# Performance work log

Hardware: AMD Instinct MI355X
Metric: run time of the kernel (lower is better)

## Reference

```python
import jax, jax.numpy as jnp
import numpy as np

B, T, D, H = 64, 1024, 512, 512
_SCALE = 1.0 / np.sqrt(H)  # torch-style RNNCell init scale


def setup_inputs() -> dict:
    key = jax.random.key(0)
    ks = jax.random.split(key, 9)
    f32 = jnp.float32
    return {
        "x": jax.random.normal(ks[0], (B, T, D), dtype=f32),
        "Wih_f": jax.random.normal(ks[1], (H, D), dtype=f32) * _SCALE,
        "Whh_f": jax.random.normal(ks[2], (H, H), dtype=f32) * _SCALE,
        "bih_f": jax.random.normal(ks[3], (H,), dtype=f32) * _SCALE,
        "bhh_f": jax.random.normal(ks[4], (H,), dtype=f32) * _SCALE,
        "Wih_b": jax.random.normal(ks[5], (H, D), dtype=f32) * _SCALE,
        "Whh_b": jax.random.normal(ks[6], (H, H), dtype=f32) * _SCALE,
        "bih_b": jax.random.normal(ks[7], (H,), dtype=f32) * _SCALE,
        "bhh_b": jax.random.normal(ks[8], (H,), dtype=f32) * _SCALE,
    }


def _scan_direction(x_bt, Wih, Whh, bih, bhh):
    # x_bt: [B, T, D] already in processing order for this direction.
    # Precompute the input projection for all timesteps (one big GEMM),
    # leaving only the recurrent GEMM inside the scan.
    xp = jnp.einsum('btd,hd->bth', x_bt, Wih) + bih + bhh  # [B, T, H]
    h0 = jnp.zeros((x_bt.shape[0], Whh.shape[0]), dtype=x_bt.dtype)

    def step(h, xt):  # xt: [B, H]
        h_new = jnp.tanh(xt + h @ Whh.T)
        return h_new, h_new

    _, hs = jax.lax.scan(step, h0, jnp.swapaxes(xp, 0, 1))  # hs: [T, B, H]
    return jnp.swapaxes(hs, 0, 1)  # [B, T, H] in processing order


def reference(x, Wih_f, Whh_f, bih_f, bhh_f, Wih_b, Whh_b, bih_b, bhh_b):
    # Forward direction: timesteps 0..T-1.
    fh = _scan_direction(x, Wih_f, Whh_f, bih_f, bhh_f)
    # Backward direction: cell consumes x reversed in time; torch code appends
    # hiddens in processing order (i.e., index t <-> original time T-1-t).
    bh = _scan_direction(x[:, ::-1, :], Wih_b, Whh_b, bih_b, bhh_b)
    # output_last=False branch: [B, 2, T, H]
    return jnp.stack([fh, bh], axis=1)
```

## Files before the change

### kernel.cpp

```cpp
#include <hip/hip_runtime.h>
#include <hip/hip_fp16.h>
#include <cstdint>

typedef _Float16 h2 __attribute__((ext_vector_type(2)));
typedef _Float16 h8 __attribute__((ext_vector_type(8)));
typedef float    f2 __attribute__((ext_vector_type(2)));
typedef float    f4 __attribute__((ext_vector_type(4)));
typedef uint32_t u4 __attribute__((ext_vector_type(4)));

#define BATCH 64
#define TSTEPS 1024
#define DDIM 512
#define HDIM 512

static __device__ __forceinline__ float fdot2(uint32_t w, uint32_t h, float acc) {
  return __builtin_amdgcn_fdot2(__builtin_bit_cast(h2, w), __builtin_bit_cast(h2, h), acc, false);
}

#define BAR_LDS()                                            \
  do {                                                       \
    __builtin_amdgcn_sched_barrier(0);                       \
    asm volatile("s_waitcnt lgkmcnt(0)" ::: "memory");       \
    __builtin_amdgcn_s_barrier();                            \
    __builtin_amdgcn_sched_barrier(0);                       \
  } while (0)

__global__ void prep_kernel(const float* __restrict__ Wih_f, const float* __restrict__ Whh_f,
                            const float* __restrict__ bih_f, const float* __restrict__ bhh_f,
                            const float* __restrict__ Wih_b, const float* __restrict__ Whh_b,
                            const float* __restrict__ bih_b, const float* __restrict__ bhh_b,
                            _Float16* __restrict__ wi16, uint32_t* __restrict__ whT,
                            float* __restrict__ bsum) {
  int i = blockIdx.x * 256 + threadIdx.x;
  if (i < 2 * 512 * 512) {
    const float* s = (i < 512 * 512) ? Wih_f : Wih_b;
    wi16[i] = (_Float16)s[i & (512 * 512 - 1)];
  }
  if (i < 2 * 256 * 512) {
    int d = i >> 17; int rem = i & ((1 << 17) - 1);
    int kp = rem >> 9; int j = rem & 511;
    const float* W = d ? Whh_b : Whh_f;
    h2 p; p[0] = (_Float16)W[j * 512 + 2 * kp]; p[1] = (_Float16)W[j * 512 + 2 * kp + 1];
    whT[i] = __builtin_bit_cast(uint32_t, p);
  }
  if (i < 2 * 512) {
    int d = i >> 9, j = i & 511;
    bsum[i] = d ? (bih_b[j] + bhh_b[j]) : (bih_f[j] + bhh_f[j]);
  }
}

__global__ __launch_bounds__(256) void xp_gemm(const float* __restrict__ x,
                                               const _Float16* __restrict__ wi,
                                               const float* __restrict__ bsum,
                                               _Float16* __restrict__ xp) {
  __shared__ _Float16 As[128][40];
  __shared__ _Float16 Bs[128][40];
  const int mt = blockIdx.x, nt = blockIdx.y, dir = blockIdx.z;
  const int m0 = mt * 128, n0 = nt * 128;
  const int tid = threadIdx.x;
  const int lane = tid & 63, w = tid >> 6;
  const int wr = w >> 1, wc = w & 1;
  const int ra = tid >> 1, hf = tid & 1;

  const int mrow = m0 + ra;
  const int bb = mrow >> 10, pp = mrow & 1023;
  const int srow = dir ? ((bb << 10) + (1023 - pp)) : mrow;
  const float*    xbase = x + (size_t)srow * 512 + hf * 16;
  const _Float16* wbase = wi + (size_t)dir * 512 * 512 + (size_t)(n0 + ra) * 512 + hf * 16;

  f4 acc[4][4];
  #pragma unroll
  for (int a = 0; a < 4; ++a)
    #pragma unroll
    for (int b = 0; b < 4; ++b) acc[a][b] = (f4)0.f;

  for (int k0 = 0; k0 < 512; k0 += 32) {
    f4 x0 = *(const f4*)(xbase + k0);
    f4 x1 = *(const f4*)(xbase + k0 + 4);
    f4 x2 = *(const f4*)(xbase + k0 + 8);
    f4 x3 = *(const f4*)(xbase + k0 + 12);
    h8 b0 = *(const h8*)(wbase + k0);
    h8 b1 = *(const h8*)(wbase + k0 + 8);
    h8 a0, a1;
    #pragma unroll
    for (int u = 0; u < 4; ++u) {
      a0[u] = (_Float16)x0[u]; a0[4 + u] = (_Float16)x1[u];
      a1[u] = (_Float16)x2[u]; a1[4 + u] = (_Float16)x3[u];
    }
    __syncthreads();
    *(h8*)&As[ra][hf * 16]     = a0;
    *(h8*)&As[ra][hf * 16 + 8] = a1;
    *(h8*)&Bs[ra][hf * 16]     = b0;
    *(h8*)&Bs[ra][hf * 16 + 8] = b1;
    __syncthreads();
    h8 af[4], bf[4];
    #pragma unroll
    for (int fm = 0; fm < 4; ++fm)
      af[fm] = *(const h8*)&As[wr * 64 + fm * 16 + (lane & 15)][(lane >> 4) * 8];
    #pragma unroll
    for (int fn = 0; fn < 4; ++fn)
      bf[fn] = *(const h8*)&Bs[wc * 64 + fn * 16 + (lane & 15)][(lane >> 4) * 8];
    #pragma unroll
    for (int fm = 0; fm < 4; ++fm)
      #pragma unroll
      for (int fn = 0; fn < 4; ++fn)
        acc[fm][fn] = __builtin_amdgcn_mfma_f32_16x16x32_f16(af[fm], bf[fn], acc[fm][fn], 0, 0, 0);
  }

  float bsv[4];
  #pragma unroll
  for (int fn = 0; fn < 4; ++fn)
    bsv[fn] = bsum[dir * 512 + n0 + wc * 64 + fn * 16 + (lane & 15)];
  #pragma unroll
  for (int fm = 0; fm < 4; ++fm)
    #pragma unroll
    for (int fn = 0; fn < 4; ++fn)
      #pragma unroll
      for (int u = 0; u < 4; ++u) {
        int m = m0 + wr * 64 + fm * 16 + (lane >> 4) * 4 + u;
        int n = n0 + wc * 64 + fn * 16 + (lane & 15);
        xp[((size_t)dir << 25) + (size_t)m * 512 + n] = (_Float16)(acc[fm][fn][u] + bsv[fn]);
      }
}

__global__ __launch_bounds__(1024, 4) void rnn_rec(const _Float16* __restrict__ xp,
                                                   const uint32_t* __restrict__ whT,
                                                   float* __restrict__ out) {
  extern __shared__ char smem[];
  uint32_t* wl   = (uint32_t*)smem;
  uint32_t* hl   = (uint32_t*)(smem + 131072);
  float*    psum = (float*)(smem + 132096);

  const int bid = blockIdx.x;
  const int dir = bid & 1, b = bid >> 1;
  const int l = threadIdx.x;
  const int w = l >> 6, lv = l & 63;
  const int ke = w >> 1, jh = w & 1;
  const int jbase = jh * 256 + lv * 4;

  const uint32_t* wb = whT + dir * (256 * 512) + (ke * 32) * 512 + jbase;
  u4 wr_[24];
  #pragma unroll
  for (int p = 0; p < 24; ++p) wr_[p] = *(const u4*)(wb + p * 512);

  char* wlb = (char*)wl + (l >> 3) * 1024 + (l & 7) * 16;
  #pragma unroll
  for (int g = 0; g < 8; ++g)
    *(u4*)(wlb + g * 128) = *(const u4*)(wb + (24 + g) * 512);

  if (l < 256) hl[l] = 0;
  __syncthreads();

  const _Float16* xpp = xp + ((size_t)dir << 25) + ((size_t)b << 19);
  float* op = out + (((size_t)(b * 2 + dir)) << 19);

  for (int t = 0; t < TSTEPS; ++t) {
    float xpv0 = 0.f, xpv1 = 0.f;
    if (l < 256) {
      h2 xv = *(const h2*)(xpp + (size_t)t * 512 + 2 * l);
      xpv0 = (float)xv[0]; xpv1 = (float)xv[1];
    }

    f4 acc = (f4)0.f;
    const uint32_t* hq = hl + ke * 32;
    #pragma unroll
    for (int cb = 0; cb < 6; ++cb) {
      u4 hv = *(const u4*)(hq + cb * 4);
      #pragma unroll
      for (int i = 0; i < 4; ++i) {
        int p = cb * 4 + i;
        #pragma unroll
        for (int jj = 0; jj < 4; ++jj) acc[jj] = fdot2(wr_[p][jj], hv[i], acc[jj]);
      }
    }
    #pragma unroll
    for (int g2 = 0; g2 < 2; ++g2) {
      u4 hv = *(const u4*)(hq + 24 + g2 * 4);
      #pragma unroll
      for (int i = 0; i < 4; ++i) {
        u4 wv = *(const u4*)(wlb + (g2 * 4 + i) * 128);
        #pragma unroll
        for (int jj = 0; jj < 4; ++jj) acc[jj] = fdot2(wv[jj], hv[i], acc[jj]);
      }
    }
    *(f4*)(psum + ke * 512 + jbase) = acc;
    BAR_LDS();

    if (l < 256) {
      float s0 = xpv0, s1 = xpv1;
      #pragma unroll
      for (int k2 = 0; k2 < 8; ++k2) {
        f2 v = *(const f2*)(psum + k2 * 512 + 2 * l);
        s0 += v[0]; s1 += v[1];
      }
      float e0 = __expf(2.f * s0);
      float h0 = 1.f - 2.f * __builtin_amdgcn_rcpf(e0 + 1.f);
      float e1 = __expf(2.f * s1);
      float h1 = 1.f - 2.f * __builtin_amdgcn_rcpf(e1 + 1.f);
      f2 o; o[0] = h0; o[1] = h1;
      *(f2*)(op + (size_t)t * 512 + 2 * l) = o;
      h2 pk; pk[0] = (_Float16)h0; pk[1] = (_Float16)h1;
      hl[l] = __builtin_bit_cast(uint32_t, pk);
    }
    BAR_LDS();
  }
}

extern "C" void kernel_launch(void* const* d_in, const int* in_sizes, int n_in,
                              void* d_out, int out_size, void* d_ws, size_t ws_size,
                              hipStream_t stream) {
  const float* x     = (const float*)d_in[0];
  const float* Wih_f = (const float*)d_in[1];
  const float* Whh_f = (const float*)d_in[2];
  const float* bih_f = (const float*)d_in[3];
  const float* bhh_f = (const float*)d_in[4];
  const float* Wih_b = (const float*)d_in[5];
  const float* Whh_b = (const float*)d_in[6];
  const float* bih_b = (const float*)d_in[7];
  const float* bhh_b = (const float*)d_in[8];

  char* ws = (char*)d_ws;
  _Float16* xp16 = (_Float16*)ws;
  _Float16* wi16 = (_Float16*)(ws + 134217728);
  uint32_t* whT  = (uint32_t*)(ws + 135266304);
  float*    bsum = (float*)(ws + 136314880);
  float* out = (float*)d_out;

  prep_kernel<<<2048, 256, 0, stream>>>(Wih_f, Whh_f, bih_f, bhh_f,
                                        Wih_b, Whh_b, bih_b, bhh_b, wi16, whT, bsum);
  dim3 g(512, 4, 2);
  xp_gemm<<<g, 256, 0, stream>>>(x, wi16, bsum, xp16);

  const int REC_LDS = 148480;
  hipFuncSetAttribute((const void*)rnn_rec, hipFuncAttributeMaxDynamicSharedMemorySize, REC_LDS);
  rnn_rec<<<128, 1024, REC_LDS, stream>>>(xp16, whT, out);
}
```

Before: 1.566 ms.

## Halve recurrent block to 512 threads with more register-resident weights per thread

The recurrent kernel moves from 1024 to 512 threads per block. Each thread now covers 8 output columns (two halves of H) and keeps 26 of its 32 k-pairs of weights in registers instead of 24, so less of the weight matrix lives in LDS and the LDS footprint shrinks. Fewer waves per block should make the two per-step barriers cheaper and cut LDS weight traffic. The cost is roughly double the serial dot-product work per thread each step and much higher register pressure, which risks spills.

```diff
diff --git a/kernel.cpp b/kernel.cpp
--- a/kernel.cpp
+++ b/kernel.cpp
@@ -123,31 +123,34 @@
       }
 }
 
-__global__ __launch_bounds__(1024, 4) void rnn_rec(const _Float16* __restrict__ xp,
-                                                   const uint32_t* __restrict__ whT,
-                                                   float* __restrict__ out) {
+__global__ __launch_bounds__(512, 2) void rnn_rec(const _Float16* __restrict__ xp,
+                                                  const uint32_t* __restrict__ whT,
+                                                  float* __restrict__ out) {
   extern __shared__ char smem[];
   uint32_t* wl   = (uint32_t*)smem;
-  uint32_t* hl   = (uint32_t*)(smem + 131072);
-  float*    psum = (float*)(smem + 132096);
+  uint32_t* hl   = (uint32_t*)(smem + 98304);
+  float*    psum = (float*)(smem + 99328);
 
   const int bid = blockIdx.x;
   const int dir = bid & 1, b = bid >> 1;
   const int l = threadIdx.x;
-  const int w = l >> 6, lv = l & 63;
-  const int ke = w >> 1, jh = w & 1;
-  const int jbase = jh * 256 + lv * 4;
-
-  const uint32_t* wb = whT + dir * (256 * 512) + (ke * 32) * 512 + jbase;
-  u4 wr_[24];
-  #pragma unroll
-  for (int p = 0; p < 24; ++p) wr_[p] = *(const u4*)(wb + p * 512);
-
-  char* wlb = (char*)wl + (l >> 3) * 1024 + (l & 7) * 16;
-  #pragma unroll
-  for (int g = 0; g < 8; ++g)
-    *(u4*)(wlb + g * 128) = *(const u4*)(wb + (24 + g) * 512);
-
+  const int ke = l >> 6, lv = l & 63;
+  const int j0 = lv * 4;
+
+  const uint32_t* wb = whT + dir * (256 * 512) + (ke * 32) * 512 + j0;
+  u4 wA[26], wB[26];
+  #pragma unroll
+  for (int p = 0; p < 26; ++p) {
+    wA[p] = *(const u4*)(wb + p * 512);
+    wB[p] = *(const u4*)(wb + p * 512 + 256);
+  }
+
+  char* wlb = (char*)wl + (l >> 3) * 1536 + (l & 7) * 16;
+  #pragma unroll
+  for (int p = 0; p < 6; ++p) {
+    *(u4*)(wlb + (p * 2 + 0) * 128) = *(const u4*)(wb + (26 + p) * 512);
+    *(u4*)(wlb + (p * 2 + 1) * 128) = *(const u4*)(wb + (26 + p) * 512 + 256);
+  }
   if (l < 256) hl[l] = 0;
   __syncthreads();
 
@@ -155,39 +158,67 @@
   float* op = out + (((size_t)(b * 2 + dir)) << 19);
 
   for (int t = 0; t < TSTEPS; ++t) {
-    float xpv0 = 0.f, xpv1 = 0.f;
-    if (l < 256) {
-      h2 xv = *(const h2*)(xpp + (size_t)t * 512 + 2 * l);
-      xpv0 = (float)xv[0]; xpv1 = (float)xv[1];
-    }
-
-    f4 acc = (f4)0.f;
+    h2 xv = (h2)(_Float16)0.f;
+    if (l < 256) xv = *(const h2*)(xpp + (size_t)t * 512 + 2 * l);
+
+    f4 aA = (f4)0.f, aB = (f4)0.f;
     const uint32_t* hq = hl + ke * 32;
+
     #pragma unroll
     for (int cb = 0; cb < 6; ++cb) {
       u4 hv = *(const u4*)(hq + cb * 4);
       #pragma unroll
       for (int i = 0; i < 4; ++i) {
-        int p = cb * 4 + i;
-        #pragma unroll
-        for (int jj = 0; jj < 4; ++jj) acc[jj] = fdot2(wr_[p][jj], hv[i], acc[jj]);
-      }
-    }
-    #pragma unroll
-    for (int g2 = 0; g2 < 2; ++g2) {
-      u4 hv = *(const u4*)(hq + 24 + g2 * 4);
-      #pragma unroll
-      for (int i = 0; i < 4; ++i) {
-        u4 wv = *(const u4*)(wlb + (g2 * 4 + i) * 128);
-        #pragma unroll
-        for (int jj = 0; jj < 4; ++jj) acc[jj] = fdot2(wv[jj], hv[i], acc[jj]);
-      }
-    }
-    *(f4*)(psum + ke * 512 + jbase) = acc;
+        const int p = cb * 4 + i;
+        #pragma unroll
+        for (int jj = 0; jj < 4; ++jj) {
+          aA[jj] = fdot2(wA[p][jj], hv[i], aA[jj]);
+          aB[jj] = fdot2(wB[p][jj], hv[i], aB[jj]);
+        }
+      }
+    }
+    {
+      u4 hv = *(const u4*)(hq + 24);
+      #pragma unroll
+      for (int i = 0; i < 2; ++i) {
+        const int p = 24 + i;
+        #pragma unroll
+        for (int jj = 0; jj < 4; ++jj) {
+          aA[jj] = fdot2(wA[p][jj], hv[i], aA[jj]);
+          aB[jj] = fdot2(wB[p][jj], hv[i], aB[jj]);
+        }
+      }
+      #pragma unroll
+      for (int p = 0; p < 2; ++p) {
+        u4 wvA = *(const u4*)(wlb + (p * 2 + 0) * 128);
+        u4 wvB = *(const u4*)(wlb + (p * 2 + 1) * 128);
+        #pragma unroll
+        for (int jj = 0; jj < 4; ++jj) {
+          aA[jj] = fdot2(wvA[jj], hv[2 + p], aA[jj]);
+          aB[jj] = fdot2(wvB[jj], hv[2 + p], aB[jj]);
+        }
+      }
+    }
+    {
+      u4 hv = *(const u4*)(hq + 28);
+      #pragma unroll
+      for (int p = 2; p < 6; ++p) {
+        u4 wvA = *(const u4*)(wlb + (p * 2 + 0) * 128);
+        u4 wvB = *(const u4*)(wlb + (p * 2 + 1) * 128);
+        #pragma unroll
+        for (int jj = 0; jj < 4; ++jj) {
+          aA[jj] = fdot2(wvA[jj], hv[p - 2], aA[jj]);
+          aB[jj] = fdot2(wvB[jj], hv[p - 2], aB[jj]);
+        }
+      }
+    }
+
+    *(f4*)(psum + ke * 512 + j0)       = aA;
+    *(f4*)(psum + ke * 512 + 256 + j0) = aB;
     BAR_LDS();
 
     if (l < 256) {
-      float s0 = xpv0, s1 = xpv1;
+      float s0 = (float)xv[0], s1 = (float)xv[1];
       #pragma unroll
       for (int k2 = 0; k2 < 8; ++k2) {
         f2 v = *(const f2*)(psum + k2 * 512 + 2 * l);
@@ -231,7 +262,7 @@
   dim3 g(512, 4, 2);
   xp_gemm<<<g, 256, 0, stream>>>(x, wi16, bsum, xp16);
 
-  const int REC_LDS = 148480;
+  const int REC_LDS = 115712;
   hipFuncSetAttribute((const void*)rnn_rec, hipFuncAttributeMaxDynamicSharedMemorySize, REC_LDS);
-  rnn_rec<<<128, 1024, REC_LDS, stream>>>(xp16, whT, out);
-}
+  rnn_rec<<<128, 512, REC_LDS, stream>>>(xp16, whT, out);
+}
```

New measurement: 1.585 ms. Within noise of the previous version (+1.2%).

## Halve recurrent block to 512 threads, stream Whh tail from global each step

Applied to the files above, without the earlier changes.

The recurrent kernel moves from 1024 to 512 threads per block. Each thread now keeps twice as many Whh columns in registers (two 24-entry halves), and the remaining 8 k-rows per half are re-read from global/L2 with volatile loads every timestep instead of from LDS. Those loads are interleaved with the fdot2 chain using sched_barriers to hide their latency. The intent is fewer waves to synchronise per barrier and a large LDS copy of the weights no longer needed. The cost is much higher register pressure and repeated global traffic on the serial critical path.

```diff
diff --git a/kernel.cpp b/kernel.cpp
--- a/kernel.cpp
+++ b/kernel.cpp
@@ -123,30 +123,26 @@
       }
 }
 
-__global__ __launch_bounds__(1024, 4) void rnn_rec(const _Float16* __restrict__ xp,
-                                                   const uint32_t* __restrict__ whT,
-                                                   float* __restrict__ out) {
-  extern __shared__ char smem[];
-  uint32_t* wl   = (uint32_t*)smem;
-  uint32_t* hl   = (uint32_t*)(smem + 131072);
-  float*    psum = (float*)(smem + 132096);
+__global__ __launch_bounds__(512, 2) void rnn_rec(const _Float16* __restrict__ xp,
+                                                  const uint32_t* __restrict__ whT,
+                                                  float* __restrict__ out) {
+  __shared__ uint32_t hl[256];
+  __shared__ float psum[8][512];
 
   const int bid = blockIdx.x;
   const int dir = bid & 1, b = bid >> 1;
   const int l = threadIdx.x;
-  const int w = l >> 6, lv = l & 63;
-  const int ke = w >> 1, jh = w & 1;
-  const int jbase = jh * 256 + lv * 4;
-
-  const uint32_t* wb = whT + dir * (256 * 512) + (ke * 32) * 512 + jbase;
-  u4 wr_[24];
-  #pragma unroll
-  for (int p = 0; p < 24; ++p) wr_[p] = *(const u4*)(wb + p * 512);
-
-  char* wlb = (char*)wl + (l >> 3) * 1024 + (l & 7) * 16;
-  #pragma unroll
-  for (int g = 0; g < 8; ++g)
-    *(u4*)(wlb + g * 128) = *(const u4*)(wb + (24 + g) * 512);
+  const int ke = l >> 6, lv = l & 63;
+  const int j0 = lv * 4;
+
+  const uint32_t* wb = whT + dir * (256 * 512) + (ke * 32) * 512 + j0;
+
+  u4 wA[24], wB[24];
+  #pragma unroll
+  for (int p = 0; p < 24; ++p) {
+    wA[p] = *(const u4*)(wb + p * 512);
+    wB[p] = *(const u4*)(wb + p * 512 + 256);
+  }
 
   if (l < 256) hl[l] = 0;
   __syncthreads();
@@ -154,43 +150,77 @@
   const _Float16* xpp = xp + ((size_t)dir << 25) + ((size_t)b << 19);
   float* op = out + (((size_t)(b * 2 + dir)) << 19);
 
+#define LDA(p)  (*(volatile const u4*)(wb + (p) * 512))
+#define LDB(p)  (*(volatile const u4*)(wb + (p) * 512 + 256))
+#define FDP(WA, WB, HW)                                   \
+  do {                                                    \
+    _Pragma("unroll")                                     \
+    for (int jj = 0; jj < 4; ++jj) {                      \
+      aA[jj] = fdot2((WA)[jj], (HW), aA[jj]);             \
+      aB[jj] = fdot2((WB)[jj], (HW), aB[jj]);             \
+    }                                                     \
+  } while (0)
+#define FD4(BASE, HV)                                     \
+  do {                                                    \
+    _Pragma("unroll")                                     \
+    for (int i = 0; i < 4; ++i)                           \
+      FDP(wA[(BASE) + i], wB[(BASE) + i], (HV)[i]);       \
+  } while (0)
+
   for (int t = 0; t < TSTEPS; ++t) {
-    float xpv0 = 0.f, xpv1 = 0.f;
+    h2 xv = (h2)(_Float16)0.f;
+    if (l < 256) xv = *(const h2*)(xpp + (size_t)t * 512 + 2 * l);
+
+    f4 aA = (f4)0.f, aB = (f4)0.f;
+    const uint32_t* hq = hl + ke * 32;
+
+    u4 sA0 = LDA(24), sB0 = LDB(24);
+    u4 sA1 = LDA(25), sB1 = LDB(25);
+    __builtin_amdgcn_sched_barrier(0x387);
+
+    { u4 hv = *(const u4*)(hq + 0); FD4(0, hv); }
+    { u4 hv = *(const u4*)(hq + 4); FD4(4, hv); }
+
+    u4 sA2 = LDA(26), sB2 = LDB(26);
+    u4 sA3 = LDA(27), sB3 = LDB(27);
+    __builtin_amdgcn_sched_barrier(0x387);
+
+    { u4 hv = *(const u4*)(hq + 8); FD4(8, hv); }
+
+    u4 hv6 = *(const u4*)(hq + 24);
+    FDP(sA0, sB0, hv6[0]);
+    FDP(sA1, sB1, hv6[1]);
+
+    u4 sA4 = LDA(28), sB4 = LDB(28);
+    u4 sA5 = LDA(29), sB5 = LDB(29);
+    __builtin_amdgcn_sched_barrier(0x387);
+
+    { u4 hv = *(const u4*)(hq + 12); FD4(12, hv); }
+    FDP(sA2, sB2, hv6[2]);
+    FDP(sA3, sB3, hv6[3]);
+
+    u4 sA6 = LDA(30), sB6 = LDB(30);
+    u4 sA7 = LDA(31), sB7 = LDB(31);
+    __builtin_amdgcn_sched_barrier(0x387);
+
+    { u4 hv = *(const u4*)(hq + 16); FD4(16, hv); }
+    u4 hv7 = *(const u4*)(hq + 28);
+    FDP(sA4, sB4, hv7[0]);
+    FDP(sA5, sB5, hv7[1]);
+
+    { u4 hv = *(const u4*)(hq + 20); FD4(20, hv); }
+    FDP(sA6, sB6, hv7[2]);
+    FDP(sA7, sB7, hv7[3]);
+
+    *(f4*)(&psum[ke][j0])       = aA;
+    *(f4*)(&psum[ke][256 + j0]) = aB;
+    BAR_LDS();
+
     if (l < 256) {
-      h2 xv = *(const h2*)(xpp + (size_t)t * 512 + 2 * l);
-      xpv0 = (float)xv[0]; xpv1 = (float)xv[1];
-    }
-
-    f4 acc = (f4)0.f;
-    const uint32_t* hq = hl + ke * 32;
-    #pragma unroll
-    for (int cb = 0; cb < 6; ++cb) {
-      u4 hv = *(const u4*)(hq + cb * 4);
-      #pragma unroll
-      for (int i = 0; i < 4; ++i) {
-        int p = cb * 4 + i;
-        #pragma unroll
-        for (int jj = 0; jj < 4; ++jj) acc[jj] = fdot2(wr_[p][jj], hv[i], acc[jj]);
-      }
-    }
-    #pragma unroll
-    for (int g2 = 0; g2 < 2; ++g2) {
-      u4 hv = *(const u4*)(hq + 24 + g2 * 4);
-      #pragma unroll
-      for (int i = 0; i < 4; ++i) {
-        u4 wv = *(const u4*)(wlb + (g2 * 4 + i) * 128);
-        #pragma unroll
-        for (int jj = 0; jj < 4; ++jj) acc[jj] = fdot2(wv[jj], hv[i], acc[jj]);
-      }
-    }
-    *(f4*)(psum + ke * 512 + jbase) = acc;
-    BAR_LDS();
-
-    if (l < 256) {
-      float s0 = xpv0, s1 = xpv1;
+      float s0 = (float)xv[0], s1 = (float)xv[1];
       #pragma unroll
       for (int k2 = 0; k2 < 8; ++k2) {
-        f2 v = *(const f2*)(psum + k2 * 512 + 2 * l);
+        f2 v = *(const f2*)(&psum[k2][2 * l]);
         s0 += v[0]; s1 += v[1];
       }
       float e0 = __expf(2.f * s0);
@@ -204,6 +234,10 @@
     }
     BAR_LDS();
   }
+#undef LDA
+#undef LDB
+#undef FDP
+#undef FD4
 }
 
 extern "C" void kernel_launch(void* const* d_in, const int* in_sizes, int n_in,
@@ -231,7 +265,5 @@
   dim3 g(512, 4, 2);
   xp_gemm<<<g, 256, 0, stream>>>(x, wi16, bsum, xp16);
 
-  const int REC_LDS = 148480;
-  hipFuncSetAttribute((const void*)rnn_rec, hipFuncAttributeMaxDynamicSharedMemorySize, REC_LDS);
-  rnn_rec<<<128, 1024, REC_LDS, stream>>>(xp16, whT, out);
-}
+  rnn_rec<<<128, 512, 0, stream>>>(xp16, whT, out);
+}
```

Result: slower. 4.952 ms (+216.2%).
